# Optimization experiments

Hardware: AMD Instinct MI355X
Metric: run time of the kernel (lower is better)

The kernel has to match this reference:

```python
import jax, jax.numpy as jnp
import numpy as np

T, H = 2048, 1024          # tokens, hidden_size
NH, NKV, D = 16, 4, 64     # heads, kv heads, head_dim
E, F = 8, 1024             # experts, intermediate_size
TOPK = 1
EPS = 1e-5
THETA = 500000.0
SCALE = D ** -0.5


def rmsnorm(x, w=None, eps=EPS):
    # fp32 accumulation like vLLM RMSNorm
    v = jnp.mean(x.astype(jnp.float32) ** 2, axis=-1, keepdims=True)
    y = x.astype(jnp.float32) * jax.lax.rsqrt(v + eps)
    y = y.astype(x.dtype)
    return y * w if w is not None else y


def setup_inputs() -> dict:
    key = jax.random.key(0)
    ks = jax.random.split(key, 12)
    s = 1.0 / np.sqrt(H)
    sf = 1.0 / np.sqrt(F)
    return {
        "positions": jnp.arange(T, dtype=jnp.int32),
        "hidden_states": jax.random.normal(ks[0], (T, H), jnp.float32),
        "ln1_w": jnp.ones((H,), jnp.float32),
        "ln2_w": jnp.ones((H,), jnp.float32),
        "wqkv": jax.random.normal(ks[1], (H, (NH + 2 * NKV) * D), jnp.float32) * s,
        "wo": jax.random.normal(ks[2], (NH * D, H), jnp.float32) * s,
        "router_w": jax.random.normal(ks[3], (H, E), jnp.float32) * s,
        "w_gate": jax.random.normal(ks[4], (E, H, F), jnp.float32) * s,
        "w_up": jax.random.normal(ks[5], (E, H, F), jnp.float32) * s,
        "w_down": jax.random.normal(ks[6], (E, F, H), jnp.float32) * sf,
        "sh_gate": jax.random.normal(ks[7], (H, F), jnp.float32) * s,
        "sh_up": jax.random.normal(ks[8], (H, F), jnp.float32) * s,
        "sh_down": jax.random.normal(ks[9], (F, H), jnp.float32) * sf,
    }


def reference(positions, hidden_states, ln1_w, ln2_w, wqkv, wo, router_w,
              w_gate, w_up, w_down, sh_gate, sh_up, sh_down):
    # --- input_layernorm (residual is None on first call) ---
    residual = hidden_states
    h = rmsnorm(hidden_states, ln1_w)

    # --- attention: qkv proj ---
    qkv = h @ wqkv
    q = qkv[:, : NH * D].reshape(T, NH, D)
    k = qkv[:, NH * D: (NH + NKV) * D].reshape(T, NKV, D)
    v = qkv[:, (NH + NKV) * D:].reshape(T, NKV, D)

    # --- neox-style RoPE ---
    half = D // 2
    inv_freq = 1.0 / (THETA ** (jnp.arange(half, dtype=jnp.float32) / half))
    ang = positions.astype(jnp.float32)[:, None] * inv_freq[None, :]
    cos = jnp.cos(ang)[:, None, :]  # [T,1,half]
    sin = jnp.sin(ang)[:, None, :]

    def rope(x):
        x1, x2 = x[..., :half], x[..., half:]
        return jnp.concatenate([x1 * cos - x2 * sin, x2 * cos + x1 * sin], axis=-1)

    q = rope(q)
    k = rope(k)

    # --- fp32 QK-RMSNorm (no weight), applied after RoPE as in source ---
    q = rmsnorm(q)
    k = rmsnorm(k)

    # --- GQA causal attention ---
    n_rep = NH // NKV
    kr = jnp.repeat(k, n_rep, axis=1)  # [T,NH,D]
    vr = jnp.repeat(v, n_rep, axis=1)
    scores = jnp.einsum('thd,shd->hts', q, kr) * SCALE  # [NH,T,T]
    causal = positions[:, None] >= positions[None, :]
    scores = jnp.where(causal[None], scores, -jnp.inf)
    attn = jax.nn.softmax(scores, axis=-1)
    ao = jnp.einsum('hts,shd->thd', attn, vr).reshape(T, NH * D)
    h = ao @ wo

    # --- post_attention_layernorm with fused residual add ---
    x = h + residual
    residual = x
    h = rmsnorm(x, ln2_w)

    # --- MoE: top-1 sigmoid router, router weight applied on input ---
    logits = h @ router_w                      # [T,E]
    score, idx = jax.lax.top_k(logits, TOPK)   # [T,1]
    gate = jax.nn.sigmoid(score.astype(jnp.float32)).astype(h.dtype)
    x_in = h * gate                            # apply_router_weight_on_input
    onehot = (idx == jnp.arange(E)[None, :]).astype(h.dtype)  # [T,E]
    g = jax.nn.silu(jnp.einsum('th,ehf->tef', x_in, w_gate)) \
        * jnp.einsum('th,ehf->tef', x_in, w_up)               # [T,E,F]
    out_e = jnp.einsum('tef,efh->teh', g, w_down)             # [T,E,H]
    routed = jnp.einsum('teh,te->th', out_e, onehot)

    # --- shared expert (SiLU MLP) ---
    shared = (jax.nn.silu(h @ sh_gate) * (h @ sh_up)) @ sh_down

    out = routed + shared
    return (out, residual)
```

## Files before the change

kernel.cpp:

```cpp
#include <hip/hip_runtime.h>
#include <hip/hip_bf16.h>
#include <cmath>
#include <cstdint>

#define T 2048
#define H 1024
#define NH 16
#define NKV 4
#define DH 64
#define NE 8
#define FF 1024
#define QKVN ((NH + 2 * NKV) * DH)
#define EPS 1e-5f
#define ATTN_SCALE 0.125f
#define LOG2E 1.44269504f
#define MBOUND 12.0f
#define ASPLIT 4

typedef short bf16x8 __attribute__((ext_vector_type(8)));
typedef float floatx4 __attribute__((ext_vector_type(4)));

__device__ __forceinline__ void gload16(const void* g, void* l) {
  __builtin_amdgcn_global_load_lds((const __attribute__((address_space(1))) void*)g,
                                   (__attribute__((address_space(3))) void*)l, 16, 0, 0);
}

__global__ __launch_bounds__(256) void rmsnorm1024(const float* __restrict__ x,
                                                   const float* __restrict__ w,
                                                   __hip_bfloat16* __restrict__ yb) {
  int row = blockIdx.x;
  const float4* x4 = (const float4*)(x + (size_t)row * H);
  float4 v = x4[threadIdx.x];
  float s = v.x * v.x + v.y * v.y + v.z * v.z + v.w * v.w;
  #pragma unroll
  for (int o = 32; o; o >>= 1) s += __shfl_down(s, o, 64);
  __shared__ float red[4];
  if ((threadIdx.x & 63) == 0) red[threadIdx.x >> 6] = s;
  __syncthreads();
  s = red[0] + red[1] + red[2] + red[3];
  float inv = rsqrtf(s * (1.0f / (float)H) + EPS);
  float4 wv = ((const float4*)w)[threadIdx.x];
  __hip_bfloat16* yp = yb + (size_t)row * H + threadIdx.x * 4;
  yp[0] = __float2bfloat16(v.x * inv * wv.x);
  yp[1] = __float2bfloat16(v.y * inv * wv.y);
  yp[2] = __float2bfloat16(v.z * inv * wv.z);
  yp[3] = __float2bfloat16(v.w * inv * wv.w);
}

__global__ __launch_bounds__(256) void fused_add_rms(const float* __restrict__ a,
                                                     const float* __restrict__ b,
                                                     float* __restrict__ resid,
                                                     const float* __restrict__ w,
                                                     float* __restrict__ yf,
                                                     __hip_bfloat16* __restrict__ yb) {
  int row = blockIdx.x;
  float4 av = ((const float4*)(a + (size_t)row * H))[threadIdx.x];
  float4 bv = ((const float4*)(b + (size_t)row * H))[threadIdx.x];
  float4 v = make_float4(av.x + bv.x, av.y + bv.y, av.z + bv.z, av.w + bv.w);
  ((float4*)(resid + (size_t)row * H))[threadIdx.x] = v;
  float s = v.x * v.x + v.y * v.y + v.z * v.z + v.w * v.w;
  #pragma unroll
  for (int o = 32; o; o >>= 1) s += __shfl_down(s, o, 64);
  __shared__ float red[4];
  if ((threadIdx.x & 63) == 0) red[threadIdx.x >> 6] = s;
  __syncthreads();
  s = red[0] + red[1] + red[2] + red[3];
  float inv = rsqrtf(s * (1.0f / (float)H) + EPS);
  float4 wv = ((const float4*)w)[threadIdx.x];
  float o0 = v.x * inv * wv.x, o1 = v.y * inv * wv.y, o2 = v.z * inv * wv.z, o3 = v.w * inv * wv.w;
  ((float4*)(yf + (size_t)row * H))[threadIdx.x] = make_float4(o0, o1, o2, o3);
  __hip_bfloat16* yp = yb + (size_t)row * H + threadIdx.x * 4;
  yp[0] = __float2bfloat16(o0);
  yp[1] = __float2bfloat16(o1);
  yp[2] = __float2bfloat16(o2);
  yp[3] = __float2bfloat16(o3);
}

__global__ __launch_bounds__(256) void tcast9(const float* __restrict__ srcE,
                                              const float* __restrict__ srcS,
                                              __hip_bfloat16* __restrict__ dst, int R, int C,
                                              long long srcStride, long long dstStride,
                                              long long sBatch, long long dBatch) {
  int z = blockIdx.z;
  const float* src = (srcS && z == (int)gridDim.z - 1) ? srcS : srcE + (long long)z * sBatch;
  dst += (long long)z * dBatch;
  int c0 = blockIdx.x * 64, r0 = blockIdx.y * 32;
  __shared__ float tile[32][65];
  int tid = threadIdx.x;
  int lr = tid >> 4;
  int lc = (tid & 15) * 4;
  #pragma unroll
  for (int it = 0; it < 2; it++) {
    float4 v = *(const float4*)(src + (long long)(r0 + lr + it * 16) * srcStride + c0 + lc);
    tile[lr + it * 16][lc + 0] = v.x;
    tile[lr + it * 16][lc + 1] = v.y;
    tile[lr + it * 16][lc + 2] = v.z;
    tile[lr + it * 16][lc + 3] = v.w;
  }
  __syncthreads();
  int oc = tid >> 2;
  int rr = (tid & 3) * 8;
  short ov[8];
  #pragma unroll
  for (int i = 0; i < 8; i++) {
    __hip_bfloat16 b = __float2bfloat16(tile[rr + i][oc]);
    ov[i] = *(short*)&b;
  }
  *(bf16x8*)((short*)dst + (long long)(c0 + oc) * dstStride + r0 + rr) = *(bf16x8*)ov;
}

__global__ __launch_bounds__(256) void gemm_bf16(const __hip_bfloat16* __restrict__ A,
                                                 const __hip_bfloat16* __restrict__ A2,
                                                 const __hip_bfloat16* __restrict__ Bt,
                                                 void* __restrict__ Cout, void* __restrict__ Cout2,
                                                 int M, int N, int K, int out_bf16,
                                                 const int* __restrict__ row_offs,
                                                 long long strideB) {
  int e = blockIdx.z;
  bool sh = (A2 != nullptr && e == (int)gridDim.z - 1);
  int rbeg = 0, rend = M;
  const __hip_bfloat16* Ap = A;
  void* Cp = Cout;
  if (sh) {
    Ap = A2; Cp = Cout2;
  } else if (row_offs) {
    rbeg = row_offs[e]; rend = row_offs[e + 1];
  }
  long long m0 = rbeg + (long long)blockIdx.y * 128;
  if (m0 >= rend) return;
  long long n0 = (long long)blockIdx.x * 64;
  const __hip_bfloat16* Bp = Bt + (long long)e * strideB;

  __shared__ unsigned short As[128 * 64];
  __shared__ unsigned short Bs[64 * 64];

  int tid = threadIdx.x;
  int lane = tid & 63, w = tid >> 6;
  int wr = (w >> 1) * 64, wc = (w & 1) * 32;
  int qd = lane >> 4, ln16 = lane & 15;
  int l7 = ln16 & 7;

  floatx4 acc[4][2];
  floatx4 zero = {0.f, 0.f, 0.f, 0.f};
  #pragma unroll
  for (int i = 0; i < 4; i++)
    #pragma unroll
    for (int j = 0; j < 2; j++) acc[i][j] = zero;

  int rowA[4], kcA[4];
  #pragma unroll
  for (int it = 0; it < 4; it++) {
    int chunk = tid + it * 256;
    rowA[it] = chunk >> 3;
    kcA[it] = ((chunk & 7) ^ (rowA[it] & 7)) * 8;
  }

  for (int k0 = 0; k0 < K; k0 += 64) {
    #pragma unroll
    for (int it = 0; it < 4; it++) {
      long long ra = m0 + rowA[it];
      if (ra >= rend) ra = rend - 1;
      gload16(Ap + ra * K + k0 + kcA[it], As + (tid + it * 256) * 8);
    }
    #pragma unroll
    for (int it = 0; it < 2; it++)
      gload16(Bp + (n0 + rowA[it]) * K + k0 + kcA[it], Bs + (tid + it * 256) * 8);
    __syncthreads();
    #pragma unroll
    for (int s = 0; s < 2; s++) {
      bf16x8 af[4], bfr[2];
      #pragma unroll
      for (int i = 0; i < 4; i++) {
        int row = wr + i * 16 + ln16;
        af[i] = *(const bf16x8*)(As + row * 64 + (((s * 4 + qd) ^ l7) * 8));
      }
      #pragma unroll
      for (int j = 0; j < 2; j++) {
        int row = wc + j * 16 + ln16;
        bfr[j] = *(const bf16x8*)(Bs + row * 64 + (((s * 4 + qd) ^ l7) * 8));
      }
      #pragma unroll
      for (int i = 0; i < 4; i++)
        #pragma unroll
        for (int j = 0; j < 2; j++)
          acc[i][j] = __builtin_amdgcn_mfma_f32_16x16x32_bf16(af[i], bfr[j], acc[i][j], 0, 0, 0);
    }
    __syncthreads();
  }

  #pragma unroll
  for (int i = 0; i < 4; i++) {
    #pragma unroll
    for (int r = 0; r < 4; r++) {
      long long gm = m0 + wr + i * 16 + qd * 4 + r;
      if (gm < rend) {
        #pragma unroll
        for (int j = 0; j < 2; j++) {
          long long gn = n0 + wc + j * 16 + ln16;
          float v = acc[i][j][r];
          if (out_bf16)
            ((__hip_bfloat16*)Cp)[gm * N + gn] = __float2bfloat16(v);
          else
            ((float*)Cp)[gm * N + gn] = v;
        }
      }
    }
  }
}

__global__ __launch_bounds__(256) void rope_pack(const float* __restrict__ qkv,
                                                 const int* __restrict__ positions,
                                                 __hip_bfloat16* __restrict__ Qb,
                                                 __hip_bfloat16* __restrict__ Kb) {
  int b = blockIdx.x * 4 + (threadIdx.x >> 6);
  int t = b / (NH + NKV);
  int hh = b % (NH + NKV);
  const float* ptr = qkv + (long long)t * QKVN + hh * DH;
  int d = threadIdx.x & 63;
  float v = ptr[d];
  int fi = d & 31;
  float inv_freq = exp2f(-(float)fi * (18.93156857f / 32.0f));
  float ang = (float)positions[t] * inv_freq;
  float c = __cosf(ang), s = __sinf(ang);
  float other = __shfl_xor(v, 32, 64);
  float r = (d < 32) ? (v * c - other * s) : (v * c + other * s);
  float sq = r * r;
  #pragma unroll
  for (int off = 32; off; off >>= 1) sq += __shfl_xor(sq, off, 64);
  float o = r * rsqrtf(sq * (1.0f / (float)DH) + EPS);
  if (hh < NH)
    Qb[(size_t)t * (NH * DH) + hh * DH + d] = __float2bfloat16(o * (ATTN_SCALE * LOG2E));
  else
    Kb[(size_t)t * (NKV * DH) + (hh - NH) * DH + d] = __float2bfloat16(o);
}

__global__ __launch_bounds__(256, 2) void attn_mfma(const __hip_bfloat16* __restrict__ Qb,
                                                    const __hip_bfloat16* __restrict__ Kb,
                                                    const __hip_bfloat16* __restrict__ VtG,
                                                    float* __restrict__ Opart,
                                                    float* __restrict__ Lpart) {
  int kvh = blockIdx.y;
  int qi = blockIdx.x;
  int sp = blockIdx.z;
  int q0 = qi * 64;
  int nt = qi + 1;
  if (sp >= nt) return;

  __shared__ unsigned short Ks[2][64 * 64];
  __shared__ unsigned short Vs[2][64 * 64];
  __shared__ unsigned short Ps[4 * 16 * 64];

  int tid = threadIdx.x;
  int lane = tid & 63, w = tid >> 6;
  int h = kvh * 4 + w;
  int qd = lane >> 4, ln16 = lane & 15;
  int l7 = ln16 & 7;
  unsigned short* Pw = Ps + w * 16 * 64;

  int r0 = tid >> 3;
  int sc = ((tid & 7) ^ (r0 & 7)) * 8;

  bf16x8 aq[4][2];
  #pragma unroll
  for (int rt = 0; rt < 4; rt++) {
    const unsigned short* qp =
        (const unsigned short*)Qb + (size_t)(q0 + rt * 16 + ln16) * (NH * DH) + h * DH;
    aq[rt][0] = *(const bf16x8*)(qp + qd * 8);
    aq[rt][1] = *(const bf16x8*)(qp + 32 + qd * 8);
  }

  bf16x8 ones;
  #pragma unroll
  for (int i = 0; i < 8; i++) ones[i] = (short)0x3F80;

  floatx4 O_[4][4], accl[4];
  floatx4 zero = {0.f, 0.f, 0.f, 0.f};
  #pragma unroll
  for (int rt = 0; rt < 4; rt++) {
    #pragma unroll
    for (int j = 0; j < 4; j++) O_[rt][j] = zero;
    accl[rt] = zero;
  }

  {
    int kb = sp * 64;
    gload16((const unsigned short*)Kb + (size_t)(kb + r0) * (NKV * DH) + kvh * DH + sc, Ks[0] + tid * 8);
    gload16((const unsigned short*)Kb + (size_t)(kb + r0 + 32) * (NKV * DH) + kvh * DH + sc, Ks[0] + tid * 8 + 2048);
    gload16((const unsigned short*)VtG + (size_t)(kvh * DH + r0) * T + kb + sc, Vs[0] + tid * 8);
    gload16((const unsigned short*)VtG + (size_t)(kvh * DH + r0 + 32) * T + kb + sc, Vs[0] + tid * 8 + 2048);
  }
  __syncthreads();

  int cur = 0;
  for (int kt = sp; kt < nt; kt += ASPLIT) {
    int ktn = kt + ASPLIT;
    if (ktn < nt) {
      int kb = ktn * 64;
      unsigned short* Kn = Ks[cur ^ 1];
      unsigned short* Vn = Vs[cur ^ 1];
      gload16((const unsigned short*)Kb + (size_t)(kb + r0) * (NKV * DH) + kvh * DH + sc, Kn + tid * 8);
      gload16((const unsigned short*)Kb + (size_t)(kb + r0 + 32) * (NKV * DH) + kvh * DH + sc, Kn + tid * 8 + 2048);
      gload16((const unsigned short*)VtG + (size_t)(kvh * DH + r0) * T + kb + sc, Vn + tid * 8);
      gload16((const unsigned short*)VtG + (size_t)(kvh * DH + r0 + 32) * T + kb + sc, Vn + tid * 8 + 2048);
    }
    const unsigned short* Kc = Ks[cur];
    const unsigned short* Vc = Vs[cur];
    int kb = kt * 64;

    #pragma unroll
    for (int rt = 0; rt < 4; rt++) {
      floatx4 S_[4];
      #pragma unroll
      for (int j = 0; j < 4; j++) S_[j] = zero;
      #pragma unroll
      for (int s = 0; s < 2; s++) {
        bf16x8 bk[4];
        #pragma unroll
        for (int j = 0; j < 4; j++)
          bk[j] = *(const bf16x8*)(Kc + (j * 16 + ln16) * 64 + (((s * 4 + qd) ^ l7) * 8));
        #pragma unroll
        for (int j = 0; j < 4; j++)
          S_[j] = __builtin_amdgcn_mfma_f32_16x16x32_bf16(aq[rt][s], bk[j], S_[j], 0, 0, 0);
      }

      int tq_base = q0 + rt * 16 + qd * 4;
      if (kb + 63 > q0 + rt * 16) {
        #pragma unroll
        for (int j = 0; j < 4; j++) {
          int tk = kb + j * 16 + ln16;
          #pragma unroll
          for (int r = 0; r < 4; r++)
            S_[j][r] = (tk <= tq_base + r) ? exp2f(S_[j][r] - MBOUND) : 0.f;
        }
      } else {
        #pragma unroll
        for (int j = 0; j < 4; j++)
          #pragma unroll
          for (int r = 0; r < 4; r++) S_[j][r] = exp2f(S_[j][r] - MBOUND);
      }

      #pragma unroll
      for (int j = 0; j < 4; j++)
        #pragma unroll
        for (int r = 0; r < 4; r++) {
          int row = qd * 4 + r;
          int pc = (((j * 2 + (ln16 >> 3)) ^ (row & 7)) * 8) + l7;
          __hip_bfloat16 pb = __float2bfloat16(S_[j][r]);
          Pw[row * 64 + pc] = *(unsigned short*)&pb;
        }

      #pragma unroll
      for (int s = 0; s < 2; s++) {
        bf16x8 ap = *(const bf16x8*)(Pw + ln16 * 64 + (((s * 4 + qd) ^ l7) * 8));
        bf16x8 bv[4];
        #pragma unroll
        for (int j = 0; j < 4; j++)
          bv[j] = *(const bf16x8*)(Vc + (j * 16 + ln16) * 64 + (((s * 4 + qd) ^ l7) * 8));
        #pragma unroll
        for (int j = 0; j < 4; j++)
          O_[rt][j] = __builtin_amdgcn_mfma_f32_16x16x32_bf16(ap, bv[j], O_[rt][j], 0, 0, 0);
        accl[rt] = __builtin_amdgcn_mfma_f32_16x16x32_bf16(ap, ones, accl[rt], 0, 0, 0);
      }
    }
    __syncthreads();
    cur ^= 1;
  }

  size_t pbase = ((size_t)(qi * NH + h) * ASPLIT + sp) * (64 * 64);
  #pragma unroll
  for (int rt = 0; rt < 4; rt++) {
    int rl_base = rt * 16 + qd * 4;
    #pragma unroll
    for (int j = 0; j < 4; j++)
      #pragma unroll
      for (int r = 0; r < 4; r++)
        Opart[pbase + (size_t)(rl_base + r) * 64 + j * 16 + ln16] = O_[rt][j][r];
  }
  if (ln16 == 0) {
    size_t lbase = ((size_t)(qi * NH + h) * ASPLIT + sp) * 64;
    #pragma unroll
    for (int rt = 0; rt < 4; rt++)
      #pragma unroll
      for (int r = 0; r < 4; r++) Lpart[lbase + rt * 16 + qd * 4 + r] = accl[rt][r];
  }
}

__global__ __launch_bounds__(256) void attn_combine(const float* __restrict__ Opart,
                                                    const float* __restrict__ Lpart,
                                                    __hip_bfloat16* __restrict__ ao) {
  int qi = blockIdx.x, h = blockIdx.y;
  int nv = (qi + 1 < ASPLIT) ? (qi + 1) : ASPLIT;
  int row = threadIdx.x >> 2;
  int c0 = (threadIdx.x & 3) * 16;
  size_t base = (size_t)(qi * NH + h) * ASPLIT * 4096;
  size_t lb = (size_t)(qi * NH + h) * ASPLIT * 64;
  float l = 0.f;
  float acc[16];
  #pragma unroll
  for (int i = 0; i < 16; i++) acc[i] = 0.f;
  for (int s = 0; s < nv; s++) {
    const float* Op = Opart + base + (size_t)s * 4096 + (size_t)row * 64 + c0;
    l += Lpart[lb + s * 64 + row];
    #pragma unroll
    for (int i = 0; i < 16; i += 4) {
      float4 v = *(const float4*)(Op + i);
      acc[i] += v.x; acc[i + 1] += v.y; acc[i + 2] += v.z; acc[i + 3] += v.w;
    }
  }
  float inv = 1.f / l;
  int t = qi * 64 + row;
  short ov[16];
  #pragma unroll
  for (int i = 0; i < 16; i++) {
    __hip_bfloat16 b = __float2bfloat16(acc[i] * inv);
    ov[i] = *(short*)&b;
  }
  short* dst = (short*)ao + (size_t)t * (NH * DH) + h * DH + c0;
  *(bf16x8*)dst = *(bf16x8*)&ov[0];
  *(bf16x8*)(dst + 8) = *(bf16x8*)&ov[8];
}

__global__ void silumul_both(const __hip_bfloat16* __restrict__ gA2,
                             const __hip_bfloat16* __restrict__ gS2,
                             __hip_bfloat16* __restrict__ gP,
                             __hip_bfloat16* __restrict__ gPs, int n4each) {
  int i = blockIdx.x * blockDim.x + threadIdx.x;
  const __hip_bfloat16* src = gA2;
  __hip_bfloat16* dst = gP;
  if (i >= n4each) {
    i -= n4each;
    src = gS2;
    dst = gPs;
  }
  int el = i * 4;
  int row = el >> 10;
  int c = el & (FF - 1);
  const __hip_bfloat16* g = src + (size_t)row * (2 * FF) + c;
  #pragma unroll
  for (int k = 0; k < 4; k++) {
    float av = __bfloat162float(g[k]);
    float bv = __bfloat162float(g[FF + k]);
    dst[el + k] = __float2bfloat16(av / (1.f + __expf(-av)) * bv);
  }
}

__global__ __launch_bounds__(64) void router_kernel(const float* __restrict__ h2,
                                                    const float* __restrict__ rw,
                                                    int* __restrict__ idx,
                                                    float* __restrict__ gate,
                                                    int* __restrict__ counts) {
  int t = blockIdx.x;
  int lane = threadIdx.x;
  float acc[NE] = {};
  for (int k = lane; k < H; k += 64) {
    float hv = h2[(long long)t * H + k];
    float4 r0 = *(const float4*)(rw + (long long)k * NE);
    float4 r1 = *(const float4*)(rw + (long long)k * NE + 4);
    acc[0] += hv * r0.x; acc[1] += hv * r0.y; acc[2] += hv * r0.z; acc[3] += hv * r0.w;
    acc[4] += hv * r1.x; acc[5] += hv * r1.y; acc[6] += hv * r1.z; acc[7] += hv * r1.w;
  }
  #pragma unroll
  for (int off = 32; off; off >>= 1)
    #pragma unroll
    for (int e2 = 0; e2 < NE; e2++) acc[e2] += __shfl_down(acc[e2], off, 64);
  if (lane == 0) {
    int best = 0;
    float bv = acc[0];
    #pragma unroll
    for (int e2 = 1; e2 < NE; e2++)
      if (acc[e2] > bv) { bv = acc[e2]; best = e2; }
    idx[t] = best;
    gate[t] = 1.f / (1.f + expf(-bv));
    atomicAdd(&counts[best], 1);
  }
}

__global__ void zero_counts_kernel(int* c) {
  if (threadIdx.x < 2 * NE) c[threadIdx.x] = 0;
}

__global__ void scan_kernel(const int* __restrict__ counts, int* __restrict__ offs) {
  if (threadIdx.x == 0) {
    int s = 0;
    for (int e2 = 0; e2 < NE; e2++) { offs[e2] = s; s += counts[e2]; }
    offs[NE] = s;
  }
}

__global__ void assign_kernel(const int* __restrict__ idx, const int* __restrict__ offs,
                              int* __restrict__ cnt2, int* __restrict__ perm,
                              int* __restrict__ pos) {
  int t = blockIdx.x * blockDim.x + threadIdx.x;
  if (t >= T) return;
  int e2 = idx[t];
  int p = offs[e2] + atomicAdd(&cnt2[e2], 1);
  pos[t] = p;
  perm[p] = t;
}

__global__ __launch_bounds__(256) void gather_kernel(const float* __restrict__ h2,
                                                     const float* __restrict__ gate,
                                                     const int* __restrict__ perm,
                                                     __hip_bfloat16* __restrict__ xg) {
  int p = blockIdx.x;
  int t = perm[p];
  float g = gate[t];
  float4 v = ((const float4*)(h2 + (long long)t * H))[threadIdx.x];
  __hip_bfloat16* yp = xg + (long long)p * H + threadIdx.x * 4;
  yp[0] = __float2bfloat16(v.x * g);
  yp[1] = __float2bfloat16(v.y * g);
  yp[2] = __float2bfloat16(v.z * g);
  yp[3] = __float2bfloat16(v.w * g);
}

__global__ __launch_bounds__(256) void final_add_kernel(float* __restrict__ out,
                                                        const float* __restrict__ outp,
                                                        const int* __restrict__ pos) {
  int t = blockIdx.x;
  int p = pos[t];
  const float4* src = (const float4*)(outp + (long long)p * H);
  float4* dst = (float4*)(out + (long long)t * H);
  float4 a = dst[threadIdx.x];
  float4 b = src[threadIdx.x];
  a.x += b.x; a.y += b.y; a.z += b.z; a.w += b.w;
  dst[threadIdx.x] = a;
}

extern "C" void kernel_launch(void* const* d_in, const int* in_sizes, int n_in,
                              void* d_out, int out_size, void* d_ws, size_t ws_size,
                              hipStream_t stream) {
  const int* positions = (const int*)d_in[0];
  const float* hidden = (const float*)d_in[1];
  const float* ln1_w = (const float*)d_in[2];
  const float* ln2_w = (const float*)d_in[3];
  const float* wqkv = (const float*)d_in[4];
  const float* wo = (const float*)d_in[5];
  const float* router_w = (const float*)d_in[6];
  const float* w_gate = (const float*)d_in[7];
  const float* w_up = (const float*)d_in[8];
  const float* w_down = (const float*)d_in[9];
  const float* sh_gate = (const float*)d_in[10];
  const float* sh_up = (const float*)d_in[11];
  const float* sh_down = (const float*)d_in[12];

  float* out = (float*)d_out;
  float* resid = out + (size_t)T * H;

  char* p = (char*)d_ws;
  auto alloc = [&](size_t bytes) { char* r = p; p += (bytes + 255) & ~(size_t)255; return r; };

  float* qkv = (float*)alloc((size_t)T * QKVN * 4);
  float* h2 = (float*)alloc((size_t)T * H * 4);
  float* gb1 = (float*)alloc((size_t)T * H * 4);
  float* outp = (float*)alloc((size_t)T * H * 4);
  __hip_bfloat16* h1b = (__hip_bfloat16*)alloc((size_t)T * H * 2);
  __hip_bfloat16* aob = (__hip_bfloat16*)alloc((size_t)T * H * 2);
  __hip_bfloat16* h2b = (__hip_bfloat16*)alloc((size_t)T * H * 2);
  __hip_bfloat16* xgb = (__hip_bfloat16*)alloc((size_t)T * H * 2);
  __hip_bfloat16* gA2 = (__hip_bfloat16*)alloc((size_t)T * 2 * FF * 2);
  __hip_bfloat16* gP = (__hip_bfloat16*)alloc((size_t)T * FF * 2);
  __hip_bfloat16* Qb = (__hip_bfloat16*)alloc((size_t)T * NH * DH * 2);
  __hip_bfloat16* Kb = (__hip_bfloat16*)alloc((size_t)T * NKV * DH * 2);
  __hip_bfloat16* VtG = (__hip_bfloat16*)alloc((size_t)NKV * DH * T * 2);
  __hip_bfloat16* wqkvT = (__hip_bfloat16*)alloc((size_t)H * QKVN * 2);
  __hip_bfloat16* woT = (__hip_bfloat16*)alloc((size_t)H * H * 2);
  __hip_bfloat16* wguT = (__hip_bfloat16*)alloc((size_t)9 * 2 * FF * H * 2);
  __hip_bfloat16* wdT = (__hip_bfloat16*)alloc((size_t)9 * H * FF * 2);
  int* counts = (int*)alloc(2 * NE * 4);
  int* cnt2 = counts + NE;
  int* offs = (int*)alloc((NE + 1) * 4);
  int* idx = (int*)alloc(T * 4);
  int* perm = (int*)alloc(T * 4);
  int* pos = (int*)alloc(T * 4);
  float* gate = (float*)alloc(T * 4);

  __hip_bfloat16* gS2 = (__hip_bfloat16*)gb1;
  __hip_bfloat16* gPs = h1b;

  float* Opart = qkv;
  float* Lpart = qkv + (size_t)(T / 64) * NH * ASPLIT * 4096;

  tcast9<<<dim3(QKVN / 64, H / 32, 1), 256, 0, stream>>>(wqkv, nullptr, wqkvT, H, QKVN, QKVN, H, 0, 0);
  tcast9<<<dim3(H / 64, H / 32, 1), 256, 0, stream>>>(wo, nullptr, woT, H, H, H, H, 0, 0);
  tcast9<<<dim3(FF / 64, H / 32, 9), 256, 0, stream>>>(w_gate, sh_gate, wguT, H, FF, FF, H,
                                                       (long long)H * FF, (long long)2 * H * FF);
  tcast9<<<dim3(FF / 64, H / 32, 9), 256, 0, stream>>>(w_up, sh_up, wguT + (size_t)FF * H, H, FF, FF, H,
                                                       (long long)H * FF, (long long)2 * H * FF);
  tcast9<<<dim3(H / 64, FF / 32, 9), 256, 0, stream>>>(w_down, sh_down, wdT, FF, H, H, FF,
                                                       (long long)FF * H, (long long)H * FF);

  rmsnorm1024<<<T, 256, 0, stream>>>(hidden, ln1_w, h1b);
  gemm_bf16<<<dim3(QKVN / 64, T / 128, 1), 256, 0, stream>>>(h1b, nullptr, wqkvT, qkv, nullptr,
                                                             T, QKVN, H, 0, nullptr, 0);
  rope_pack<<<T * (NH + NKV) / 4, 256, 0, stream>>>(qkv, positions, Qb, Kb);
  tcast9<<<dim3(NKV * DH / 64, T / 32, 1), 256, 0, stream>>>(qkv + (NH + NKV) * DH, nullptr, VtG,
                                                             T, NKV * DH, QKVN, T, 0, 0);
  attn_mfma<<<dim3(T / 64, NKV, ASPLIT), 256, 0, stream>>>(Qb, Kb, VtG, Opart, Lpart);
  attn_combine<<<dim3(T / 64, NH), 256, 0, stream>>>(Opart, Lpart, aob);
  gemm_bf16<<<dim3(H / 64, T / 128, 1), 256, 0, stream>>>(aob, nullptr, woT, gb1, nullptr,
                                                          T, H, H, 0, nullptr, 0);
  fused_add_rms<<<T, 256, 0, stream>>>(gb1, hidden, resid, ln2_w, h2, h2b);
  zero_counts_kernel<<<1, 64, 0, stream>>>(counts);
  router_kernel<<<T, 64, 0, stream>>>(h2, router_w, idx, gate, counts);
  scan_kernel<<<1, 64, 0, stream>>>(counts, offs);
  assign_kernel<<<T / 256, 256, 0, stream>>>(idx, offs, cnt2, perm, pos);
  gather_kernel<<<T, 256, 0, stream>>>(h2, gate, perm, xgb);
  gemm_bf16<<<dim3(2 * FF / 64, T / 128, 9), 256, 0, stream>>>(xgb, h2b, wguT, gA2, gS2,
                                                               T, 2 * FF, H, 1, offs,
                                                               (long long)2 * H * FF);
  silumul_both<<<(2 * T * FF / 4) / 256, 256, 0, stream>>>(gA2, gS2, gP, gPs, T * FF / 4);
  gemm_bf16<<<dim3(H / 64, T / 128, 9), 256, 0, stream>>>(gP, gPs, wdT, outp, out,
                                                          T, H, FF, 0, offs, (long long)FF * H);
  final_add_kernel<<<T, 256, 0, stream>>>(out, outp, pos);
}
```

Measured before the change: 409.3 us.

## Triple-buffer GEMM and attention loads, fuse gather into expert GEMM, merge routing kernels

The GEMM and attention kernels move from a single or double LDS buffer to a three-slot ring. Tiles are prefetched two steps ahead and waited on with explicit vmcnt waits and raw barriers, so global-to-LDS loads overlap with MFMA work. The routed-expert GEMM now reads h2b rows through the permutation and applies the sigmoid gate in its epilogue, which removes the separate gather kernel and its buffer. Zeroing the counts moves into fused_add_rms, and scan and assign merge into one single-block kernel. The costs are three times the LDS footprint, which may lower occupancy, a gate scale applied after bf16 rounding of the input rather than before, and a serial assign loop in one block.

```diff
diff --git a/kernel.cpp b/kernel.cpp
--- a/kernel.cpp
+++ b/kernel.cpp
@@ -20,6 +20,8 @@
 typedef short bf16x8 __attribute__((ext_vector_type(8)));
 typedef float floatx4 __attribute__((ext_vector_type(4)));
 
+#define VMCNT(n) asm volatile("s_waitcnt vmcnt(" #n ")" ::: "memory")
+
 __device__ __forceinline__ void gload16(const void* g, void* l) {
   __builtin_amdgcn_global_load_lds((const __attribute__((address_space(1))) void*)g,
                                    (__attribute__((address_space(3))) void*)l, 16, 0, 0);
@@ -52,8 +54,10 @@
                                                      float* __restrict__ resid,
                                                      const float* __restrict__ w,
                                                      float* __restrict__ yf,
-                                                     __hip_bfloat16* __restrict__ yb) {
+                                                     __hip_bfloat16* __restrict__ yb,
+                                                     int* __restrict__ counts_g) {
   int row = blockIdx.x;
+  if (row == 0 && threadIdx.x < 2 * NE) counts_g[threadIdx.x] = 0;
   float4 av = ((const float4*)(a + (size_t)row * H))[threadIdx.x];
   float4 bv = ((const float4*)(b + (size_t)row * H))[threadIdx.x];
   float4 v = make_float4(av.x + bv.x, av.y + bv.y, av.z + bv.z, av.w + bv.w);
@@ -115,14 +119,17 @@
                                                  void* __restrict__ Cout, void* __restrict__ Cout2,
                                                  int M, int N, int K, int out_bf16,
                                                  const int* __restrict__ row_offs,
-                                                 long long strideB) {
+                                                 long long strideB,
+                                                 const int* __restrict__ permA,
+                                                 const float* __restrict__ gatev) {
   int e = blockIdx.z;
   bool sh = (A2 != nullptr && e == (int)gridDim.z - 1);
   int rbeg = 0, rend = M;
   const __hip_bfloat16* Ap = A;
   void* Cp = Cout;
+  const int* pA = permA;
   if (sh) {
-    Ap = A2; Cp = Cout2;
+    Ap = A2; Cp = Cout2; pA = nullptr;
   } else if (row_offs) {
     rbeg = row_offs[e]; rend = row_offs[e + 1];
   }
@@ -131,8 +138,8 @@
   long long n0 = (long long)blockIdx.x * 64;
   const __hip_bfloat16* Bp = Bt + (long long)e * strideB;
 
-  __shared__ unsigned short As[128 * 64];
-  __shared__ unsigned short Bs[64 * 64];
+  __shared__ unsigned short As[3 * 128 * 64];
+  __shared__ unsigned short Bs[3 * 64 * 64];
 
   int tid = threadIdx.x;
   int lane = tid & 63, w = tid >> 6;
@@ -148,36 +155,58 @@
     for (int j = 0; j < 2; j++) acc[i][j] = zero;
 
   int rowA[4], kcA[4];
+  const unsigned short* Arow[4];
+  const unsigned short* Brow[2];
   #pragma unroll
   for (int it = 0; it < 4; it++) {
     int chunk = tid + it * 256;
     rowA[it] = chunk >> 3;
     kcA[it] = ((chunk & 7) ^ (rowA[it] & 7)) * 8;
-  }
-
-  for (int k0 = 0; k0 < K; k0 += 64) {
-    #pragma unroll
-    for (int it = 0; it < 4; it++) {
-      long long ra = m0 + rowA[it];
-      if (ra >= rend) ra = rend - 1;
-      gload16(Ap + ra * K + k0 + kcA[it], As + (tid + it * 256) * 8);
-    }
+    long long ra = m0 + rowA[it];
+    if (ra >= rend) ra = rend - 1;
+    long long tok = pA ? (long long)pA[ra] : ra;
+    Arow[it] = (const unsigned short*)Ap + tok * K;
+  }
+  #pragma unroll
+  for (int it = 0; it < 2; it++)
+    Brow[it] = (const unsigned short*)Bp + (n0 + rowA[it]) * K;
+
+  auto stage = [&](int j) {
+    int slot = j % 3;
+    int kk = j << 6;
+    unsigned short* Ad = As + slot * 8192;
+    unsigned short* Bd = Bs + slot * 4096;
+    #pragma unroll
+    for (int it = 0; it < 4; it++)
+      gload16(Arow[it] + kk + kcA[it], Ad + (tid + it * 256) * 8);
     #pragma unroll
     for (int it = 0; it < 2; it++)
-      gload16(Bp + (n0 + rowA[it]) * K + k0 + kcA[it], Bs + (tid + it * 256) * 8);
-    __syncthreads();
+      gload16(Brow[it] + kk + kcA[it], Bd + (tid + it * 256) * 8);
+  };
+
+  int NT = K >> 6;
+  stage(0);
+  if (NT > 1) { stage(1); VMCNT(6); } else { VMCNT(0); }
+  __builtin_amdgcn_s_barrier();
+  __builtin_amdgcn_sched_barrier(0);
+
+  for (int k = 0; k < NT; k++) {
+    if (k + 2 < NT) stage(k + 2);
+    __builtin_amdgcn_sched_barrier(0);
+    const unsigned short* Ac = As + (k % 3) * 8192;
+    const unsigned short* Bc = Bs + (k % 3) * 4096;
     #pragma unroll
     for (int s = 0; s < 2; s++) {
       bf16x8 af[4], bfr[2];
       #pragma unroll
       for (int i = 0; i < 4; i++) {
         int row = wr + i * 16 + ln16;
-        af[i] = *(const bf16x8*)(As + row * 64 + (((s * 4 + qd) ^ l7) * 8));
+        af[i] = *(const bf16x8*)(Ac + row * 64 + (((s * 4 + qd) ^ l7) * 8));
       }
       #pragma unroll
       for (int j = 0; j < 2; j++) {
         int row = wc + j * 16 + ln16;
-        bfr[j] = *(const bf16x8*)(Bs + row * 64 + (((s * 4 + qd) ^ l7) * 8));
+        bfr[j] = *(const bf16x8*)(Bc + row * 64 + (((s * 4 + qd) ^ l7) * 8));
       }
       #pragma unroll
       for (int i = 0; i < 4; i++)
@@ -185,7 +214,11 @@
         for (int j = 0; j < 2; j++)
           acc[i][j] = __builtin_amdgcn_mfma_f32_16x16x32_bf16(af[i], bfr[j], acc[i][j], 0, 0, 0);
     }
-    __syncthreads();
+    if (k + 1 < NT) {
+      if (k + 2 < NT) { VMCNT(6); } else { VMCNT(0); }
+      __builtin_amdgcn_s_barrier();
+      __builtin_amdgcn_sched_barrier(0);
+    }
   }
 
   #pragma unroll
@@ -194,10 +227,12 @@
     for (int r = 0; r < 4; r++) {
       long long gm = m0 + wr + i * 16 + qd * 4 + r;
       if (gm < rend) {
+        float gsc = 1.0f;
+        if (pA && gatev) gsc = gatev[pA[gm]];
         #pragma unroll
         for (int j = 0; j < 2; j++) {
           long long gn = n0 + wc + j * 16 + ln16;
-          float v = acc[i][j][r];
+          float v = acc[i][j][r] * gsc;
           if (out_bf16)
             ((__hip_bfloat16*)Cp)[gm * N + gn] = __float2bfloat16(v);
           else
@@ -235,7 +270,7 @@
 }
 
 __global__ __launch_bounds__(256, 2) void attn_mfma(const __hip_bfloat16* __restrict__ Qb,
-                                                    const __hip_bfloat16* __restrict__ Kb,
+                                                    const __hip_bfloat16* __restrict__ Kbuf,
                                                     const __hip_bfloat16* __restrict__ VtG,
                                                     float* __restrict__ Opart,
                                                     float* __restrict__ Lpart) {
@@ -245,9 +280,10 @@
   int q0 = qi * 64;
   int nt = qi + 1;
   if (sp >= nt) return;
-
-  __shared__ unsigned short Ks[2][64 * 64];
-  __shared__ unsigned short Vs[2][64 * 64];
+  int NT = (nt - 1 - sp) / ASPLIT + 1;
+
+  __shared__ unsigned short Ks[3 * 64 * 64];
+  __shared__ unsigned short Vs[3 * 64 * 64];
   __shared__ unsigned short Ps[4 * 16 * 64];
 
   int tid = threadIdx.x;
@@ -260,6 +296,20 @@
   int r0 = tid >> 3;
   int sc = ((tid & 7) ^ (r0 & 7)) * 8;
 
+  const unsigned short* KbP = (const unsigned short*)Kbuf;
+  const unsigned short* VtP = (const unsigned short*)VtG;
+
+  auto stage = [&](int k) {
+    int kb = (sp + k * ASPLIT) * 64;
+    int slot = k % 3;
+    unsigned short* Kd = Ks + slot * 4096;
+    unsigned short* Vd = Vs + slot * 4096;
+    gload16(KbP + (size_t)(kb + r0) * (NKV * DH) + kvh * DH + sc, Kd + tid * 8);
+    gload16(KbP + (size_t)(kb + r0 + 32) * (NKV * DH) + kvh * DH + sc, Kd + tid * 8 + 2048);
+    gload16(VtP + (size_t)(kvh * DH + r0) * T + kb + sc, Vd + tid * 8);
+    gload16(VtP + (size_t)(kvh * DH + r0 + 32) * T + kb + sc, Vd + tid * 8 + 2048);
+  };
+
   bf16x8 aq[4][2];
   #pragma unroll
   for (int rt = 0; rt < 4; rt++) {
@@ -282,30 +332,17 @@
     accl[rt] = zero;
   }
 
-  {
-    int kb = sp * 64;
-    gload16((const unsigned short*)Kb + (size_t)(kb + r0) * (NKV * DH) + kvh * DH + sc, Ks[0] + tid * 8);
-    gload16((const unsigned short*)Kb + (size_t)(kb + r0 + 32) * (NKV * DH) + kvh * DH + sc, Ks[0] + tid * 8 + 2048);
-    gload16((const unsigned short*)VtG + (size_t)(kvh * DH + r0) * T + kb + sc, Vs[0] + tid * 8);
-    gload16((const unsigned short*)VtG + (size_t)(kvh * DH + r0 + 32) * T + kb + sc, Vs[0] + tid * 8 + 2048);
-  }
-  __syncthreads();
-
-  int cur = 0;
-  for (int kt = sp; kt < nt; kt += ASPLIT) {
-    int ktn = kt + ASPLIT;
-    if (ktn < nt) {
-      int kb = ktn * 64;
-      unsigned short* Kn = Ks[cur ^ 1];
-      unsigned short* Vn = Vs[cur ^ 1];
-      gload16((const unsigned short*)Kb + (size_t)(kb + r0) * (NKV * DH) + kvh * DH + sc, Kn + tid * 8);
-      gload16((const unsigned short*)Kb + (size_t)(kb + r0 + 32) * (NKV * DH) + kvh * DH + sc, Kn + tid * 8 + 2048);
-      gload16((const unsigned short*)VtG + (size_t)(kvh * DH + r0) * T + kb + sc, Vn + tid * 8);
-      gload16((const unsigned short*)VtG + (size_t)(kvh * DH + r0 + 32) * T + kb + sc, Vn + tid * 8 + 2048);
-    }
-    const unsigned short* Kc = Ks[cur];
-    const unsigned short* Vc = Vs[cur];
-    int kb = kt * 64;
+  stage(0);
+  if (NT > 1) { stage(1); VMCNT(4); } else { VMCNT(0); }
+  __builtin_amdgcn_s_barrier();
+  __builtin_amdgcn_sched_barrier(0);
+
+  for (int k = 0; k < NT; k++) {
+    if (k + 2 < NT) stage(k + 2);
+    __builtin_amdgcn_sched_barrier(0);
+    const unsigned short* Kc = Ks + (k % 3) * 4096;
+    const unsigned short* Vc = Vs + (k % 3) * 4096;
+    int kb = (sp + k * ASPLIT) * 64;
 
     #pragma unroll
     for (int rt = 0; rt < 4; rt++) {
@@ -362,8 +399,11 @@
         accl[rt] = __builtin_amdgcn_mfma_f32_16x16x32_bf16(ap, ones, accl[rt], 0, 0, 0);
       }
     }
-    __syncthreads();
-    cur ^= 1;
+    if (k + 1 < NT) {
+      if (k + 2 < NT) { VMCNT(4); } else { VMCNT(0); }
+      __builtin_amdgcn_s_barrier();
+      __builtin_amdgcn_sched_barrier(0);
+    }
   }
 
   size_t pbase = ((size_t)(qi * NH + h) * ASPLIT + sp) * (64 * 64);
@@ -475,42 +515,25 @@
   }
 }
 
-__global__ void zero_counts_kernel(int* c) {
-  if (threadIdx.x < 2 * NE) c[threadIdx.x] = 0;
-}
-
-__global__ void scan_kernel(const int* __restrict__ counts, int* __restrict__ offs) {
+__global__ __launch_bounds__(256) void assign_scan(const int* __restrict__ counts,
+                                                   const int* __restrict__ idx,
+                                                   int* __restrict__ offs,
+                                                   int* __restrict__ cnt2,
+                                                   int* __restrict__ perm,
+                                                   int* __restrict__ pos) {
+  __shared__ int offs_s[NE + 1];
   if (threadIdx.x == 0) {
     int s = 0;
-    for (int e2 = 0; e2 < NE; e2++) { offs[e2] = s; s += counts[e2]; }
-    offs[NE] = s;
-  }
-}
-
-__global__ void assign_kernel(const int* __restrict__ idx, const int* __restrict__ offs,
-                              int* __restrict__ cnt2, int* __restrict__ perm,
-                              int* __restrict__ pos) {
-  int t = blockIdx.x * blockDim.x + threadIdx.x;
-  if (t >= T) return;
-  int e2 = idx[t];
-  int p = offs[e2] + atomicAdd(&cnt2[e2], 1);
-  pos[t] = p;
-  perm[p] = t;
-}
-
-__global__ __launch_bounds__(256) void gather_kernel(const float* __restrict__ h2,
-                                                     const float* __restrict__ gate,
-                                                     const int* __restrict__ perm,
-                                                     __hip_bfloat16* __restrict__ xg) {
-  int p = blockIdx.x;
-  int t = perm[p];
-  float g = gate[t];
-  float4 v = ((const float4*)(h2 + (long long)t * H))[threadIdx.x];
-  __hip_bfloat16* yp = xg + (long long)p * H + threadIdx.x * 4;
-  yp[0] = __float2bfloat16(v.x * g);
-  yp[1] = __float2bfloat16(v.y * g);
-  yp[2] = __float2bfloat16(v.z * g);
-  yp[3] = __float2bfloat16(v.w * g);
+    for (int e2 = 0; e2 < NE; e2++) { offs_s[e2] = s; offs[e2] = s; s += counts[e2]; }
+    offs_s[NE] = s; offs[NE] = s;
+  }
+  __syncthreads();
+  for (int t = threadIdx.x; t < T; t += 256) {
+    int e2 = idx[t];
+    int p = offs_s[e2] + atomicAdd(&cnt2[e2], 1);
+    pos[t] = p;
+    perm[p] = t;
+  }
 }
 
 __global__ __launch_bounds__(256) void final_add_kernel(float* __restrict__ out,
@@ -556,7 +579,6 @@
   __hip_bfloat16* h1b = (__hip_bfloat16*)alloc((size_t)T * H * 2);
   __hip_bfloat16* aob = (__hip_bfloat16*)alloc((size_t)T * H * 2);
   __hip_bfloat16* h2b = (__hip_bfloat16*)alloc((size_t)T * H * 2);
-  __hip_bfloat16* xgb = (__hip_bfloat16*)alloc((size_t)T * H * 2);
   __hip_bfloat16* gA2 = (__hip_bfloat16*)alloc((size_t)T * 2 * FF * 2);
   __hip_bfloat16* gP = (__hip_bfloat16*)alloc((size_t)T * FF * 2);
   __hip_bfloat16* Qb = (__hip_bfloat16*)alloc((size_t)T * NH * DH * 2);
@@ -591,25 +613,23 @@
 
   rmsnorm1024<<<T, 256, 0, stream>>>(hidden, ln1_w, h1b);
   gemm_bf16<<<dim3(QKVN / 64, T / 128, 1), 256, 0, stream>>>(h1b, nullptr, wqkvT, qkv, nullptr,
-                                                             T, QKVN, H, 0, nullptr, 0);
+                                                             T, QKVN, H, 0, nullptr, 0, nullptr, nullptr);
   rope_pack<<<T * (NH + NKV) / 4, 256, 0, stream>>>(qkv, positions, Qb, Kb);
   tcast9<<<dim3(NKV * DH / 64, T / 32, 1), 256, 0, stream>>>(qkv + (NH + NKV) * DH, nullptr, VtG,
                                                              T, NKV * DH, QKVN, T, 0, 0);
   attn_mfma<<<dim3(T / 64, NKV, ASPLIT), 256, 0, stream>>>(Qb, Kb, VtG, Opart, Lpart);
   attn_combine<<<dim3(T / 64, NH), 256, 0, stream>>>(Opart, Lpart, aob);
   gemm_bf16<<<dim3(H / 64, T / 128, 1), 256, 0, stream>>>(aob, nullptr, woT, gb1, nullptr,
-                                                          T, H, H, 0, nullptr, 0);
-  fused_add_rms<<<T, 256, 0, stream>>>(gb1, hidden, resid, ln2_w, h2, h2b);
-  zero_counts_kernel<<<1, 64, 0, stream>>>(counts);
+                                                          T, H, H, 0, nullptr, 0, nullptr, nullptr);
+  fused_add_rms<<<T, 256, 0, stream>>>(gb1, hidden, resid, ln2_w, h2, h2b, counts);
   router_kernel<<<T, 64, 0, stream>>>(h2, router_w, idx, gate, counts);
-  scan_kernel<<<1, 64, 0, stream>>>(counts, offs);
-  assign_kernel<<<T / 256, 256, 0, stream>>>(idx, offs, cnt2, perm, pos);
-  gather_kernel<<<T, 256, 0, stream>>>(h2, gate, perm, xgb);
-  gemm_bf16<<<dim3(2 * FF / 64, T / 128, 9), 256, 0, stream>>>(xgb, h2b, wguT, gA2, gS2,
+  assign_scan<<<1, 256, 0, stream>>>(counts, idx, offs, cnt2, perm, pos);
+  gemm_bf16<<<dim3(2 * FF / 64, T / 128, 9), 256, 0, stream>>>(h2b, h2b, wguT, gA2, gS2,
                                                                T, 2 * FF, H, 1, offs,
-                                                               (long long)2 * H * FF);
+                                                               (long long)2 * H * FF, perm, gate);
   silumul_both<<<(2 * T * FF / 4) / 256, 256, 0, stream>>>(gA2, gS2, gP, gPs, T * FF / 4);
   gemm_bf16<<<dim3(H / 64, T / 128, 9), 256, 0, stream>>>(gP, gPs, wdT, outp, out,
-                                                          T, H, FF, 0, offs, (long long)FF * H);
+                                                          T, H, FF, 0, offs, (long long)FF * H,
+                                                          nullptr, nullptr);
   final_add_kernel<<<T, 256, 0, stream>>>(out, outp, pos);
 }
```

Result: slower. 432.3 us (+5.6%).
